# Optimization experiments

Hardware: AMD Instinct MI355X
Metric: run time of the kernel (lower is better)

The kernel has to match this reference:

```python
import jax, jax.numpy as jnp
import numpy as np

NUM_EMBEDDINGS = 8192
EMBEDDING_DIM = 512
BATCH = 16384
COMMITMENT_COST = 0.25
EMBEDDING_SCALE = 0.1


def setup_inputs() -> dict:
    key = jax.random.key(0)
    k1, k2 = jax.random.split(key)
    x = jax.random.randint(k1, (BATCH,), 0, NUM_EMBEDDINGS, dtype=jnp.int64 if jax.config.jax_enable_x64 else jnp.int32)
    # codebook initialized uniform(-scale, scale) like the torch module
    W = jax.random.uniform(k2, (NUM_EMBEDDINGS, EMBEDDING_DIM), dtype=jnp.float32,
                           minval=-EMBEDDING_SCALE, maxval=EMBEDDING_SCALE)
    return {"x": x, "W": W}


def reference(x, W):
    # x: (B,) int indices into codebook; W: (K, D) codebook
    x_emb = W[x]                                           # (B, D) gather
    # squared euclidean distances via ||a||^2 + ||b||^2 - 2 a.b  -> (B, K)
    distances = ((x_emb ** 2).sum(axis=1, keepdims=True)
                 + (W ** 2).sum(axis=1)
                 - 2.0 * jnp.einsum('bd,kd->bk', x_emb, W))
    assignments = jnp.argmin(distances, axis=1)            # (B,)
    quantized = W[assignments]                             # (B, D)
    diff = quantized - x_emb                               # (B, D)
    loss = (diff ** 2).sum(axis=1).mean()
    loss = loss + COMMITMENT_COST * (W ** 2).sum()
    return (loss, quantized, diff)
```

## Files before the change

kernel.cpp:

```cpp
#include <hip/hip_runtime.h>

#define NUM_EMB    8192
#define EMB_DIM    512
#define BATCH_N    16384
#define BD         (BATCH_N * EMB_DIM)
#define TOTAL_OUT  (2 * BD + 1)
#define NCHUNK     (TOTAL_OUT / 4)
#define QCHUNK_END (BD / 4)
#define NBLOCKS    2048
#define NTHREADS   256
#define NTOTAL     (NBLOCKS * NTHREADS)

__device__ float g_partial[NBLOCKS];

__global__ __launch_bounds__(NTHREADS) void vq_sum(const float* __restrict__ W) {
    int tid = blockIdx.x * NTHREADS + threadIdx.x;
    const float4* W4 = (const float4*)W;
    float4 a = W4[tid];
    float4 b = W4[tid + NTOTAL];
    float s = a.x*a.x + a.y*a.y + a.z*a.z + a.w*a.w
            + b.x*b.x + b.y*b.y + b.z*b.z + b.w*b.w;
#pragma unroll
    for (int off = 32; off > 0; off >>= 1) s += __shfl_down(s, off, 64);
    __shared__ float ls[NTHREADS / 64];
    if ((threadIdx.x & 63) == 0) ls[threadIdx.x >> 6] = s;
    __syncthreads();
    if (threadIdx.x == 0) g_partial[blockIdx.x] = ls[0] + ls[1] + ls[2] + ls[3];
}

__global__ __launch_bounds__(NTHREADS) void vq_write(const int* __restrict__ x,
        const float* __restrict__ W, float* __restrict__ out) {
    const int tid  = blockIdx.x * NTHREADS + threadIdx.x;
    const int lane = threadIdx.x & 63;
    const int wave = (tid >> 6);
    float4* out4 = (float4*)out;

    const int b0 = 2 * wave;
    const int b1 = 2 * wave + 1;

    int k0 = x[b0];
    int k1 = x[b1];
    int kp = (b0 > 0) ? x[b0 - 1] : 0;

#pragma unroll
    for (int k = 0; k < 4; ++k) {
        int c = QCHUNK_END + 1 + tid + k * NTOTAL;
        if (c < NCHUNK) out4[c] = make_float4(0.f, 0.f, 0.f, 0.f);
    }
    if (blockIdx.x == 1 && threadIdx.x == 0) {
        out[TOTAL_OUT - 1] = 0.0f;
        float w = W[x[BATCH_N - 1] * EMB_DIM + 511];
        out4[QCHUNK_END] = make_float4(w, 0.f, 0.f, 0.f);
    }

    const float4* R0 = (const float4*)(W + k0 * EMB_DIM);
    const float4* R1 = (const float4*)(W + k1 * EMB_DIM);
    float4 a0 = R0[2 * lane], a1 = R0[2 * lane + 1];
    float4 c0 = R1[2 * lane], c1 = R1[2 * lane + 1];
    float p0 = W[kp * EMB_DIM + 511];
    float p1 = W[k0 * EMB_DIM + 511];

    {
        float pw = __shfl_up(a1.w, 1, 64);
        float first = (lane == 0) ? p0 : pw;
        int cb = 128 * b0;
        if (b0 != 0 || lane != 0)
            out4[cb + 2 * lane]     = make_float4(first, a0.x, a0.y, a0.z);
        out4[cb + 2 * lane + 1]     = make_float4(a0.w,  a1.x, a1.y, a1.z);
    }
    {
        float pw = __shfl_up(c1.w, 1, 64);
        float first = (lane == 0) ? p1 : pw;
        int cb = 128 * b1;
        out4[cb + 2 * lane]         = make_float4(first, c0.x, c0.y, c0.z);
        out4[cb + 2 * lane + 1]     = make_float4(c0.w,  c1.x, c1.y, c1.z);
    }

    if (blockIdx.x == 0) {
        __shared__ float red[NTHREADS];
        float s = 0.0f;
        for (int i = threadIdx.x; i < NBLOCKS; i += NTHREADS) s += g_partial[i];
        red[threadIdx.x] = s;
        __syncthreads();
        for (int st = NTHREADS / 2; st > 0; st >>= 1) {
            if (threadIdx.x < st) red[threadIdx.x] += red[threadIdx.x + st];
            __syncthreads();
        }
        if (threadIdx.x == 0) {
            float loss = 0.25f * red[0];
            int k = x[0];
            float4 v = *(const float4*)(W + k * EMB_DIM);
            out4[0] = make_float4(loss, v.x, v.y, v.z);
        }
    }
}

extern "C" void kernel_launch(void* const* d_in, const int* in_sizes, int n_in,
                              void* d_out, int out_size, void* d_ws, size_t ws_size,
                              hipStream_t stream) {
    const int*   x = (const int*)d_in[0];
    const float* W = (const float*)d_in[1];
    float* out     = (float*)d_out;

    vq_sum<<<NBLOCKS, NTHREADS, 0, stream>>>(W);
    vq_write<<<NBLOCKS, NTHREADS, 0, stream>>>(x, W, out);
}
```

Measured before the change: 94.65 us.

## Fuse codebook-norm and output-write kernels into one cooperative kernel with grid sync

Merges the sum-of-squares reduction kernel and the gather/write kernel into a single kernel launched with hipLaunchCooperativeKernel, using a grid-wide sync between the reduction and the writes. The block count is halved, and each thread now reads four W float4s for the reduction while each wave writes four gathered rows, carrying the shifted boundary element between rows with shuffles. This removes one kernel launch and its inter-kernel gap. In exchange it adds a grid barrier and cooperative-launch overhead, and it relies on all 1024 blocks being co-resident.

```diff
diff --git a/kernel.cpp b/kernel.cpp
--- a/kernel.cpp
+++ b/kernel.cpp
@@ -1,4 +1,7 @@
 #include <hip/hip_runtime.h>
+#include <hip/hip_cooperative_groups.h>
+
+namespace cg = cooperative_groups;
 
 #define NUM_EMB    8192
 #define EMB_DIM    512
@@ -7,43 +10,27 @@
 #define TOTAL_OUT  (2 * BD + 1)
 #define NCHUNK     (TOTAL_OUT / 4)
 #define QCHUNK_END (BD / 4)
-#define NBLOCKS    2048
+#define NBLOCKS    1024
 #define NTHREADS   256
 #define NTOTAL     (NBLOCKS * NTHREADS)
 
 __device__ float g_partial[NBLOCKS];
 
-__global__ __launch_bounds__(NTHREADS) void vq_sum(const float* __restrict__ W) {
-    int tid = blockIdx.x * NTHREADS + threadIdx.x;
-    const float4* W4 = (const float4*)W;
-    float4 a = W4[tid];
-    float4 b = W4[tid + NTOTAL];
-    float s = a.x*a.x + a.y*a.y + a.z*a.z + a.w*a.w
-            + b.x*b.x + b.y*b.y + b.z*b.z + b.w*b.w;
-#pragma unroll
-    for (int off = 32; off > 0; off >>= 1) s += __shfl_down(s, off, 64);
-    __shared__ float ls[NTHREADS / 64];
-    if ((threadIdx.x & 63) == 0) ls[threadIdx.x >> 6] = s;
-    __syncthreads();
-    if (threadIdx.x == 0) g_partial[blockIdx.x] = ls[0] + ls[1] + ls[2] + ls[3];
-}
-
-__global__ __launch_bounds__(NTHREADS) void vq_write(const int* __restrict__ x,
-        const float* __restrict__ W, float* __restrict__ out) {
+__global__ __launch_bounds__(NTHREADS, 4) void vq_coop(
+        const int* __restrict__ x, const float* __restrict__ W,
+        float* __restrict__ out) {
     const int tid  = blockIdx.x * NTHREADS + threadIdx.x;
     const int lane = threadIdx.x & 63;
-    const int wave = (tid >> 6);
     float4* out4 = (float4*)out;
+    const float4* W4 = (const float4*)W;
 
-    const int b0 = 2 * wave;
-    const int b1 = 2 * wave + 1;
-
-    int k0 = x[b0];
-    int k1 = x[b1];
-    int kp = (b0 > 0) ? x[b0 - 1] : 0;
+    float4 a0 = W4[tid];
+    float4 a1 = W4[tid +     NTOTAL];
+    float4 a2 = W4[tid + 2 * NTOTAL];
+    float4 a3 = W4[tid + 3 * NTOTAL];
 
 #pragma unroll
-    for (int k = 0; k < 4; ++k) {
+    for (int k = 0; k < 8; ++k) {
         int c = QCHUNK_END + 1 + tid + k * NTOTAL;
         if (c < NCHUNK) out4[c] = make_float4(0.f, 0.f, 0.f, 0.f);
     }
@@ -53,34 +40,74 @@
         out4[QCHUNK_END] = make_float4(w, 0.f, 0.f, 0.f);
     }
 
-    const float4* R0 = (const float4*)(W + k0 * EMB_DIM);
-    const float4* R1 = (const float4*)(W + k1 * EMB_DIM);
-    float4 a0 = R0[2 * lane], a1 = R0[2 * lane + 1];
-    float4 c0 = R1[2 * lane], c1 = R1[2 * lane + 1];
-    float p0 = W[kp * EMB_DIM + 511];
-    float p1 = W[k0 * EMB_DIM + 511];
+    float s = a0.x*a0.x + a0.y*a0.y + a0.z*a0.z + a0.w*a0.w
+            + a1.x*a1.x + a1.y*a1.y + a1.z*a1.z + a1.w*a1.w
+            + a2.x*a2.x + a2.y*a2.y + a2.z*a2.z + a2.w*a2.w
+            + a3.x*a3.x + a3.y*a3.y + a3.z*a3.z + a3.w*a3.w;
+#pragma unroll
+    for (int off = 32; off > 0; off >>= 1) s += __shfl_down(s, off, 64);
+    __shared__ float ls[NTHREADS / 64];
+    if (lane == 0) ls[threadIdx.x >> 6] = s;
+    __syncthreads();
+    if (threadIdx.x == 0) g_partial[blockIdx.x] = ls[0] + ls[1] + ls[2] + ls[3];
+
+    cg::this_grid().sync();
 
     {
-        float pw = __shfl_up(a1.w, 1, 64);
-        float first = (lane == 0) ? p0 : pw;
-        int cb = 128 * b0;
-        if (b0 != 0 || lane != 0)
-            out4[cb + 2 * lane]     = make_float4(first, a0.x, a0.y, a0.z);
-        out4[cb + 2 * lane + 1]     = make_float4(a0.w,  a1.x, a1.y, a1.z);
-    }
-    {
-        float pw = __shfl_up(c1.w, 1, 64);
-        float first = (lane == 0) ? p1 : pw;
-        int cb = 128 * b1;
-        out4[cb + 2 * lane]         = make_float4(first, c0.x, c0.y, c0.z);
-        out4[cb + 2 * lane + 1]     = make_float4(c0.w,  c1.x, c1.y, c1.z);
+        const int wave = tid >> 6;
+        const int base = 4 * wave;
+        int kp = (base > 0) ? x[base - 1] : 0;
+        int r0 = x[base], r1 = x[base + 1], r2 = x[base + 2], r3 = x[base + 3];
+        float prev = W[kp * EMB_DIM + 511];
+
+        const float4* R0 = (const float4*)(W + r0 * EMB_DIM);
+        const float4* R1 = (const float4*)(W + r1 * EMB_DIM);
+        const float4* R2 = (const float4*)(W + r2 * EMB_DIM);
+        const float4* R3 = (const float4*)(W + r3 * EMB_DIM);
+        float4 f0a = R0[2*lane], f0b = R0[2*lane+1];
+        float4 f1a = R1[2*lane], f1b = R1[2*lane+1];
+        float4 f2a = R2[2*lane], f2b = R2[2*lane+1];
+        float4 f3a = R3[2*lane], f3b = R3[2*lane+1];
+
+        {
+            float pw = __shfl_up(f0b.w, 1, 64);
+            float first = (lane == 0) ? prev : pw;
+            int cb = 128 * base;
+            if (base != 0 || lane != 0)
+                out4[cb + 2*lane] = make_float4(first, f0a.x, f0a.y, f0a.z);
+            out4[cb + 2*lane + 1] = make_float4(f0a.w, f0b.x, f0b.y, f0b.z);
+            prev = __shfl(f0b.w, 63, 64);
+        }
+        {
+            float pw = __shfl_up(f1b.w, 1, 64);
+            float first = (lane == 0) ? prev : pw;
+            int cb = 128 * (base + 1);
+            out4[cb + 2*lane]     = make_float4(first, f1a.x, f1a.y, f1a.z);
+            out4[cb + 2*lane + 1] = make_float4(f1a.w, f1b.x, f1b.y, f1b.z);
+            prev = __shfl(f1b.w, 63, 64);
+        }
+        {
+            float pw = __shfl_up(f2b.w, 1, 64);
+            float first = (lane == 0) ? prev : pw;
+            int cb = 128 * (base + 2);
+            out4[cb + 2*lane]     = make_float4(first, f2a.x, f2a.y, f2a.z);
+            out4[cb + 2*lane + 1] = make_float4(f2a.w, f2b.x, f2b.y, f2b.z);
+            prev = __shfl(f2b.w, 63, 64);
+        }
+        {
+            float pw = __shfl_up(f3b.w, 1, 64);
+            float first = (lane == 0) ? prev : pw;
+            int cb = 128 * (base + 3);
+            out4[cb + 2*lane]     = make_float4(first, f3a.x, f3a.y, f3a.z);
+            out4[cb + 2*lane + 1] = make_float4(f3a.w, f3b.x, f3b.y, f3b.z);
+        }
     }
 
     if (blockIdx.x == 0) {
         __shared__ float red[NTHREADS];
-        float s = 0.0f;
-        for (int i = threadIdx.x; i < NBLOCKS; i += NTHREADS) s += g_partial[i];
-        red[threadIdx.x] = s;
+        float t = 0.0f;
+        for (int i = threadIdx.x; i < NBLOCKS; i += NTHREADS) t += g_partial[i];
+        red[threadIdx.x] = t;
         __syncthreads();
         for (int st = NTHREADS / 2; st > 0; st >>= 1) {
             if (threadIdx.x < st) red[threadIdx.x] += red[threadIdx.x + st];
@@ -102,6 +129,7 @@
     const float* W = (const float*)d_in[1];
     float* out     = (float*)d_out;
 
-    vq_sum<<<NBLOCKS, NTHREADS, 0, stream>>>(W);
-    vq_write<<<NBLOCKS, NTHREADS, 0, stream>>>(x, W, out);
+    void* args[] = { (void*)&x, (void*)&W, (void*)&out };
+    hipLaunchCooperativeKernel((void*)vq_coop, dim3(NBLOCKS), dim3(NTHREADS),
+                               args, 0, stream);
 }
```

Result: slower. 229.1 us (+142.0%).
